# Kernel tuning notes

Measured on AMD Instinct MI355X. Metric: run time of the kernel, lower is better.

## Reference

```python
import jax, jax.numpy as jnp
import numpy as np

B, K, G = 1048576, 32, 8
SIGMA = 1.0


def setup_inputs() -> dict:
    key = jax.random.key(0)
    k1, k2 = jax.random.split(key)
    mu = jax.random.normal(k1, (B, K), dtype=jnp.float32)
    private_attribute = jax.random.randint(k2, (B,), 0, G, dtype=jnp.int64 if jax.config.jax_enable_x64 else jnp.int32)
    return {"mu": mu, "private_attribute": private_attribute}


def _gmm_loss(mu, labels):
    # --- segment reduce: per-label counts, means, covariances ---
    onehot = jax.nn.one_hot(labels, G, dtype=mu.dtype)          # [B,G]
    counts = jnp.sum(onehot, axis=0)                             # [G]
    mu_g = (onehot.T @ mu) / counts[:, None]                     # [G,K] group means
    diff = mu - mu_g[labels]                                     # [B,K] centered rows
    # Sigma_sum[g] = sum_{i in g} diff_i^T diff_i  (outer products)
    sigma_sum = jnp.einsum('bg,bi,bj->gij', onehot, diff, diff)  # [G,K,K]
    eye = jnp.eye(K, dtype=mu.dtype)
    sigma_g = SIGMA * eye + sigma_sum / counts[:, None, None]    # [G,K,K]

    # --- per-group inverse / logdet for Gaussian KL ---
    inv = jnp.linalg.inv(sigma_g)                                # [G,K,K]
    _, logdet = jnp.linalg.slogdet(sigma_g)                      # [G]

    # --- pairwise KL( N(u_i,S_i) || N(u_j,S_j) ) ---
    # tr(S_j^{-1} S_i)
    tr = jnp.einsum('jab,iba->ij', inv, sigma_g)                 # [G,G]
    d = mu_g[None, :, :] - mu_g[:, None, :]                      # d[i,j] = u_j - u_i
    mahal = jnp.einsum('ijd,jde,ije->ij', d, inv, d)             # [G,G]
    kl = 0.5 * (tr + mahal - K + logdet[None, :] - logdet[:, None])

    # original loop: for i in range(G-1): for j in range(1, G): if j != i
    idx = jnp.arange(G)
    mask = (idx[:, None] < G - 1) & (idx[None, :] >= 1) & (idx[:, None] != idx[None, :])
    w = counts[:, None] * counts[None, :]
    result = jnp.sum(jnp.where(mask, kl * w, jnp.zeros_like(kl)))
    return result / (float(B) ** 2)


def reference(mu, private_attribute):
    return _gmm_loss(mu, private_attribute)
```

## Files before the change

### kernel.cpp

```cpp
#include <hip/hip_runtime.h>
#include <math.h>

#define K 32
#define G 8
#define SIGMA_V 1.0f
#define RF __builtin_amdgcn_readfirstlane
#define RPB 512
#define RPW 128

#define RAW_OFF   0
#define MUSUM_OFF 8192
#define CNT_OFF   8448
#define ICNT_OFF  8456
#define CUR_OFF   8464
#define DESC_OFF  8480
#define IDX_OFF   16384
#define HDR_INTS  16384

#define WAITV(n) asm volatile("s_waitcnt vmcnt(" #n ")" ::: "memory")
typedef __attribute__((address_space(3))) void lds_void;
typedef __attribute__((address_space(1))) void glb_void;
#define GLL(gsrc, ldst) __builtin_amdgcn_global_load_lds((const glb_void*)(gsrc), (lds_void*)(ldst), 16, 0, 0)

__global__ __launch_bounds__(256, 8) void gmm_hist(const int* __restrict__ lab,
                                                   int* __restrict__ wsI, int B) {
  __shared__ int h[G];
  if (threadIdx.x < G) h[threadIdx.x] = 0;
  __syncthreads();
  int c[G];
  #pragma unroll
  for (int g = 0; g < G; ++g) c[g] = 0;
  const int nt = gridDim.x * blockDim.x;
  const int4* lab4 = reinterpret_cast<const int4*>(lab);
  for (int i = blockIdx.x * blockDim.x + threadIdx.x; i < B / 4; i += nt) {
    const int4 v = lab4[i];
    #pragma unroll
    for (int g = 0; g < G; ++g)
      c[g] += (v.x == g) + (v.y == g) + (v.z == g) + (v.w == g);
  }
  const int lane = threadIdx.x & 63;
  #pragma unroll
  for (int g = 0; g < G; ++g) {
    int t = c[g];
    #pragma unroll
    for (int off = 32; off >= 1; off >>= 1) t += __shfl_xor(t, off);
    if (lane == 0) atomicAdd(&h[g], t);
  }
  __syncthreads();
  if (threadIdx.x < G) atomicAdd(&wsI[ICNT_OFF + threadIdx.x], h[threadIdx.x]);
}

__global__ void gmm_prep(float* __restrict__ ws, int* __restrict__ wsI, int B, int nblk) {
  __shared__ int off[G], bb[G + 1], scnt[G];
  const int tid = threadIdx.x;
  if (tid == 0) {
    int o = 0, b = 0;
    for (int g = 0; g < G; ++g) {
      const int c = wsI[ICNT_OFF + g];
      scnt[g] = c; off[g] = o; bb[g] = b;
      ws[CNT_OFF + g] = (float)c;
      wsI[CUR_OFF + g] = o;
      o = (o + c + 15) & ~15;
      b += (c + RPB - 1) / RPB;
    }
    bb[G] = b;
  }
  __syncthreads();
  for (int t = tid; t < nblk; t += blockDim.x) {
    int st = 0, cn = 0, gg = 0;
    #pragma unroll
    for (int g = 0; g < G; ++g) {
      if (t >= bb[g] && t < bb[g + 1]) {
        const int k = t - bb[g];
        st = off[g] + k * RPB;
        const int rem = scnt[g] - k * RPB;
        cn = rem < RPB ? rem : RPB;
        gg = g;
      }
    }
    wsI[DESC_OFF + 3 * t]     = st;
    wsI[DESC_OFF + 3 * t + 1] = cn;
    wsI[DESC_OFF + 3 * t + 2] = gg;
  }
}

__global__ __launch_bounds__(256, 8) void gmm_scatter(const int* __restrict__ lab,
                                                      int* __restrict__ wsI, int B) {
  __shared__ int lcnt[G], lbase[G], lpos[G];
  const int tid = threadIdx.x;
  const int base = blockIdx.x * 1024;
  if (tid < G) { lcnt[tid] = 0; lpos[tid] = 0; }
  __syncthreads();
  const int4 v = *reinterpret_cast<const int4*>(lab + base + tid * 4);
  atomicAdd(&lcnt[v.x], 1); atomicAdd(&lcnt[v.y], 1);
  atomicAdd(&lcnt[v.z], 1); atomicAdd(&lcnt[v.w], 1);
  __syncthreads();
  if (tid < G) lbase[tid] = atomicAdd(&wsI[CUR_OFF + tid], lcnt[tid]);
  __syncthreads();
  int p;
  p = atomicAdd(&lpos[v.x], 1); wsI[IDX_OFF + lbase[v.x] + p] = base + tid * 4;
  p = atomicAdd(&lpos[v.y], 1); wsI[IDX_OFF + lbase[v.y] + p] = base + tid * 4 + 1;
  p = atomicAdd(&lpos[v.z], 1); wsI[IDX_OFF + lbase[v.z] + p] = base + tid * 4 + 2;
  p = atomicAdd(&lpos[v.w], 1); wsI[IDX_OFF + lbase[v.w] + p] = base + tid * 4 + 3;
}

#define OUTER(a, b) { \
  acc[0]=fmaf(a.x,b.x,acc[0]);   acc[1]=fmaf(a.x,b.y,acc[1]);   acc[2]=fmaf(a.x,b.z,acc[2]);   acc[3]=fmaf(a.x,b.w,acc[3]); \
  acc[4]=fmaf(a.y,b.x,acc[4]);   acc[5]=fmaf(a.y,b.y,acc[5]);   acc[6]=fmaf(a.y,b.z,acc[6]);   acc[7]=fmaf(a.y,b.w,acc[7]); \
  acc[8]=fmaf(a.z,b.x,acc[8]);   acc[9]=fmaf(a.z,b.y,acc[9]);   acc[10]=fmaf(a.z,b.z,acc[10]); acc[11]=fmaf(a.z,b.w,acc[11]); \
  acc[12]=fmaf(a.w,b.x,acc[12]); acc[13]=fmaf(a.w,b.y,acc[13]); acc[14]=fmaf(a.w,b.z,acc[14]); acc[15]=fmaf(a.w,b.w,acc[15]); \
  if (i8 == 0) { ms[0]+=b.x; ms[1]+=b.y; ms[2]+=b.z; ms[3]+=b.w; } }

#define STAGE(vlo, vhi, b) do { \
  float* db = &lds[wave * 1024 + (b) * 512]; \
  GLL(mu + (size_t)(unsigned)(vlo) * K + lf * 4, db); \
  GLL(mu + (size_t)(unsigned)(vhi) * K + lf * 4, db + 256); \
} while (0)

#define COMPUTE(b) do { \
  const float* sb = &lds[wave * 1024 + (b) * 512]; \
  _Pragma("unroll") \
  for (int r = 0; r < 16; ++r) { \
    const float4 a = *reinterpret_cast<const float4*>(&sb[r * 32 + i8 * 4]); \
    const float4 bv = *reinterpret_cast<const float4*>(&sb[r * 32 + j8 * 4]); \
    OUTER(a, bv); \
  } \
} while (0)

__global__ __launch_bounds__(256, 4) void gmm_stats3(const float* __restrict__ mu,
                                                     const int* __restrict__ wsI,
                                                     float* __restrict__ ws) {
  __shared__ float lds[4224];
  const int bd  = blockIdx.x * 3;
  const int s   = RF(wsI[DESC_OFF + bd]);
  const int cnt = RF(wsI[DESC_OFF + bd + 1]);
  const int g   = RF(wsI[DESC_OFF + bd + 2]);
  if (cnt <= 0) return;

  const int tid = threadIdx.x, wave = tid >> 6, lane = tid & 63;
  const int i8 = lane >> 3, j8 = lane & 7;
  const int lg = lane >> 3, lf = lane & 7;
  float acc[16], ms[4];
  #pragma unroll
  for (int e = 0; e < 16; ++e) acc[e] = 0.f;
  ms[0] = ms[1] = ms[2] = ms[3] = 0.f;

  int wcnt = cnt - wave * RPW;
  wcnt = wcnt < 0 ? 0 : (wcnt > RPW ? RPW : wcnt);
  const int* idxp = wsI + IDX_OFF + s + wave * RPW;

  const int nch = wcnt >> 4;
  int alo = 0, ahi = 0, slo = 0, shi = 0, tlo = 0, thi = 0;
  if (nch > 0) { alo = idxp[lg]; ahi = idxp[8 + lg]; }
  if (nch > 1) { slo = idxp[16 + lg]; shi = idxp[24 + lg]; }
  if (nch > 0) {
    if (nch > 1) WAITV(2); else WAITV(0);
    STAGE(alo, ahi, 0);
  }
  int buf = 0;
  for (int k = 0; k < nch; ++k) {
    const bool h1 = (k + 1) < nch, h2 = (k + 2) < nch;
    if (h2) { tlo = idxp[(k + 2) * 16 + lg]; thi = idxp[(k + 2) * 16 + 8 + lg]; }
    if (h1) {
      if (h2) { WAITV(4); } else { WAITV(2); }
      STAGE(slo, shi, buf ^ 1);
      if (h2) { WAITV(4); } else { WAITV(2); }
    } else {
      WAITV(0);
    }
    COMPUTE(buf);
    slo = tlo; shi = thi;
    buf ^= 1;
  }
  for (int q = nch << 4; q < wcnt; ++q) {
    const int r = idxp[q];
    const float* rp = mu + (size_t)(unsigned)r * K;
    const float4 a = *reinterpret_cast<const float4*>(rp + i8 * 4);
    const float4 bv = *reinterpret_cast<const float4*>(rp + j8 * 4);
    OUTER(a, bv);
  }

  __syncthreads();
  #pragma unroll
  for (int e = 0; e < 16; ++e) lds[wave * 1056 + e * 64 + lane] = acc[e];
  if (i8 == 0) {
    #pragma unroll
    for (int e = 0; e < 4; ++e) lds[wave * 1056 + 1024 + j8 * 4 + e] = ms[e];
  }
  __syncthreads();
  for (int t = tid; t < 1056; t += 256) {
    const float sm = lds[t] + lds[1056 + t] + lds[2112 + t] + lds[3168 + t];
    if (t < 1024) {
      const int e = t >> 6, ln = t & 63;
      const int row = 4 * (ln >> 3) + (e >> 2), col = 4 * (ln & 7) + (e & 3);
      atomicAdd(ws + RAW_OFF + g * K * K + row * K + col, sm);
    } else {
      atomicAdd(ws + MUSUM_OFF + g * K + (t - 1024), sm);
    }
  }
}

#define ACC_CASE(gc_, Av, Bv_) do{ \
  facc[gc_][0]=fmaf(Av.x,Bv_.x,facc[gc_][0]); facc[gc_][1]=fmaf(Av.x,Bv_.y,facc[gc_][1]); \
  facc[gc_][2]=fmaf(Av.y,Bv_.x,facc[gc_][2]); facc[gc_][3]=fmaf(Av.y,Bv_.y,facc[gc_][3]); \
  if (a_blk==0){ msum[gc_][0]+=Bv_.x; msum[gc_][1]+=Bv_.y; } }while(0)
#define PROC(gv, Av, Bv_) switch(gv){ \
  case 0: ACC_CASE(0,Av,Bv_); break; case 1: ACC_CASE(1,Av,Bv_); break; \
  case 2: ACC_CASE(2,Av,Bv_); break; case 3: ACC_CASE(3,Av,Bv_); break; \
  case 4: ACC_CASE(4,Av,Bv_); break; case 5: ACC_CASE(5,Av,Bv_); break; \
  case 6: ACC_CASE(6,Av,Bv_); break; default: ACC_CASE(7,Av,Bv_); break; }

__global__ __launch_bounds__(256, 4) void gmm_stats_fb(const float* __restrict__ mu,
                                                       const int* __restrict__ lab,
                                                       float* __restrict__ ws, int B) {
  const int tid = threadIdx.x;
  const int a_blk = tid >> 4, b_blk = tid & 15;
  const int rpb = B / 1024;
  const long rbase = (long)blockIdx.x * rpb;
  float facc[G][4]; float msum[G][2];
  #pragma unroll
  for (int g = 0; g < G; ++g) { facc[g][0]=facc[g][1]=facc[g][2]=facc[g][3]=0.f; msum[g][0]=msum[g][1]=0.f; }
  const float2* __restrict__ mu2 = reinterpret_cast<const float2*>(mu);
  for (int q = 0; q < rpb; ++q) {
    const long r = rbase + q;
    const float2 Av = mu2[r * 16 + a_blk];
    const float2 Bv_ = mu2[r * 16 + b_blk];
    const int g0 = RF(lab[r]);
    PROC(g0, Av, Bv_);
  }
  const int arow = a_blk * 2, bcol = b_blk * 2;
  #pragma unroll
  for (int g = 0; g < G; ++g) {
    float* base = &ws[RAW_OFF + g * K * K];
    atomicAdd(base + (arow)*K + bcol, facc[g][0]);
    atomicAdd(base + (arow)*K + bcol + 1, facc[g][1]);
    atomicAdd(base + (arow+1)*K + bcol, facc[g][2]);
    atomicAdd(base + (arow+1)*K + bcol + 1, facc[g][3]);
  }
  if (a_blk == 0)
    #pragma unroll
    for (int g = 0; g < G; ++g) {
      atomicAdd(&ws[MUSUM_OFF + g*K + bcol], msum[g][0]);
      atomicAdd(&ws[MUSUM_OFF + g*K + bcol + 1], msum[g][1]);
    }
}

__global__ __launch_bounds__(512, 1) void gmm_finalize(const float* __restrict__ ws,
                                                       float* __restrict__ out, int B) {
  __shared__ double sig[G][K][K];
  __shared__ double inv[G][K][K];
  __shared__ double mg[G][K];
  __shared__ double ldet[G];
  __shared__ double cshared[G];
  __shared__ double pairsum[G];
  const int tid = threadIdx.x;
  const int w = tid >> 6;
  const int lane = tid & 63;

  if (tid < G) cshared[tid] = (double)ws[CNT_OFF + tid];
  __syncthreads();
  const double cinv = 1.0 / cshared[w];
  if (lane < K) mg[w][lane] = (double)ws[MUSUM_OFF + w * K + lane] * cinv;
  __syncthreads();
  for (int e = lane; e < K * K; e += 64) {
    const int a = e >> 5, b = e & 31;
    double s = (double)ws[RAW_OFF + w * K * K + e] * cinv - mg[w][a] * mg[w][b];
    if (a == b) s += (double)SIGMA_V;
    sig[w][a][b] = s;
  }
  __syncthreads();

  const int c = lane & 31;
  double col[K];
  #pragma unroll
  for (int i2 = 0; i2 < K; ++i2) {
    double sv = sig[w][i2][c];
    col[i2] = (lane < K) ? sv : ((i2 == c) ? 1.0 : 0.0);
  }
  double ld = 0.0;
  #pragma unroll
  for (int j2 = 0; j2 < K; ++j2) {
    double rowj = col[j2];
    double p = __shfl(rowj, j2);
    double pinv = 1.0 / p;
    ld += log(p);
    double scaled = rowj * pinv;
    #pragma unroll
    for (int i2 = 0; i2 < K; ++i2) {
      if (i2 == j2) continue;
      double bij = __shfl(col[i2], j2);
      col[i2] = fma(-bij, scaled, col[i2]);
    }
    col[j2] = scaled;
  }
  if (lane >= K) {
    #pragma unroll
    for (int i2 = 0; i2 < K; ++i2) inv[w][i2][lane - K] = col[i2];
  }
  if (lane == 0) ldet[w] = ld;
  __syncthreads();

  double accp = 0.0;
  for (int jj = 0; jj < G; ++jj) {
    const bool ok = (w < G - 1) && (jj >= 1) && (w != jj);
    if (ok) {
      double t = 0.0;
      for (int e = lane; e < K * K; e += 64) {
        const int a = e >> 5, b = e & 31;
        const double da = mg[jj][a] - mg[w][a];
        const double db = mg[jj][b] - mg[w][b];
        t += inv[jj][a][b] * (sig[w][a][b] + da * db);
      }
      #pragma unroll
      for (int off = 32; off >= 1; off >>= 1) t += __shfl_xor(t, off);
      if (lane == 0) accp += 0.5 * (t - (double)K + ldet[jj] - ldet[w]) * cshared[w] * cshared[jj];
    }
  }
  if (lane == 0) pairsum[w] = accp;
  __syncthreads();
  if (tid == 0) {
    double tot = 0.0;
    #pragma unroll
    for (int q = 0; q < G; ++q) tot += pairsum[q];
    const double Bf = (double)B;
    out[0] = (float)(tot / (Bf * Bf));
  }
}

extern "C" void kernel_launch(void* const* d_in, const int* in_sizes, int n_in,
                              void* d_out, int out_size, void* d_ws, size_t ws_size,
                              hipStream_t stream) {
  const float* mu = (const float*)d_in[0];
  const int* lab = (const int*)d_in[1];
  float* ws = (float*)d_ws;
  int* wsI = (int*)d_ws;
  float* out = (float*)d_out;
  const int B = in_sizes[1];

  hipMemsetAsync(d_ws, 0, (size_t)DESC_OFF * 4, stream);
  hipLaunchKernelGGL(gmm_hist, dim3(256), dim3(256), 0, stream, lab, wsI, B);

  const size_t need = (size_t)(HDR_INTS + B + 16 * G + 32) * 4;
  if (ws_size >= need) {
    const int nblk = (B + RPB - 1) / RPB + G;
    hipLaunchKernelGGL(gmm_prep, dim3(1), dim3(256), 0, stream, ws, wsI, B, nblk);
    hipLaunchKernelGGL(gmm_scatter, dim3(B / 1024), dim3(256), 0, stream, lab, wsI, B);
    hipLaunchKernelGGL(gmm_stats3, dim3(nblk), dim3(256), 0, stream, mu, wsI, ws);
  } else {
    hipLaunchKernelGGL(gmm_prep, dim3(1), dim3(256), 0, stream, ws, wsI, B, 0);
    hipLaunchKernelGGL(gmm_stats_fb, dim3(1024), dim3(256), 0, stream, mu, lab, ws, B);
  }
  hipLaunchKernelGGL(gmm_finalize, dim3(1), dim3(512), 0, stream, ws, out, B);
}
```

Baseline: 209.9 us.

## Fuse prep into histogram, locally sort scatter output, deepen stats pipeline

The single-block prep kernel is folded into the histogram kernel: the last block to finish, found with an atomic done counter, computes offsets and block descriptors, which removes one launch. The scatter kernel now sorts indices per group in LDS before writing, so global writes are contiguous runs instead of random single stores. The stats kernel switches to 8-row chunks with a 4-deep global_load_lds ring buffer on the full-chunk path and accumulates mean sums in every lane rather than only i8==0. The partial-chunk path now waits on each load before using it, which serialises loads, and the change in ms accumulation has to stay consistent with how those sums are reduced later.

Result: slower. 219.0 us (+4.3%).

```diff
diff --git a/kernel.cpp b/kernel.cpp
--- a/kernel.cpp
+++ b/kernel.cpp
@@ -13,6 +13,7 @@
 #define CNT_OFF   8448
 #define ICNT_OFF  8456
 #define CUR_OFF   8464
+#define DONE_OFF  8472
 #define DESC_OFF  8480
 #define IDX_OFF   16384
 #define HDR_INTS  16384
@@ -23,45 +24,52 @@
 #define GLL(gsrc, ldst) __builtin_amdgcn_global_load_lds((const glb_void*)(gsrc), (lds_void*)(ldst), 16, 0, 0)
 
 __global__ __launch_bounds__(256, 8) void gmm_hist(const int* __restrict__ lab,
-                                                   int* __restrict__ wsI, int B) {
+                                                   float* __restrict__ ws,
+                                                   int* __restrict__ wsI, int B, int nblk) {
   __shared__ int h[G];
-  if (threadIdx.x < G) h[threadIdx.x] = 0;
+  __shared__ int amLast;
+  __shared__ int off[G], bb[G + 1], scnt[G];
+  const int tid = threadIdx.x;
+  if (tid < G) h[tid] = 0;
   __syncthreads();
   int c[G];
   #pragma unroll
   for (int g = 0; g < G; ++g) c[g] = 0;
   const int nt = gridDim.x * blockDim.x;
   const int4* lab4 = reinterpret_cast<const int4*>(lab);
-  for (int i = blockIdx.x * blockDim.x + threadIdx.x; i < B / 4; i += nt) {
+  for (int i = blockIdx.x * blockDim.x + tid; i < B / 4; i += nt) {
     const int4 v = lab4[i];
     #pragma unroll
     for (int g = 0; g < G; ++g)
       c[g] += (v.x == g) + (v.y == g) + (v.z == g) + (v.w == g);
   }
-  const int lane = threadIdx.x & 63;
+  const int lane = tid & 63;
   #pragma unroll
   for (int g = 0; g < G; ++g) {
     int t = c[g];
     #pragma unroll
-    for (int off = 32; off >= 1; off >>= 1) t += __shfl_xor(t, off);
+    for (int o = 32; o >= 1; o >>= 1) t += __shfl_xor(t, o);
     if (lane == 0) atomicAdd(&h[g], t);
   }
   __syncthreads();
-  if (threadIdx.x < G) atomicAdd(&wsI[ICNT_OFF + threadIdx.x], h[threadIdx.x]);
-}
-
-__global__ void gmm_prep(float* __restrict__ ws, int* __restrict__ wsI, int B, int nblk) {
-  __shared__ int off[G], bb[G + 1], scnt[G];
-  const int tid = threadIdx.x;
+  if (tid < G) atomicAdd(&wsI[ICNT_OFF + tid], h[tid]);
+  __syncthreads();
+  if (tid == 0) {
+    __threadfence();
+    amLast = (atomicAdd(&wsI[DONE_OFF], 1) == (int)gridDim.x - 1);
+  }
+  __syncthreads();
+  if (!amLast) return;
+
   if (tid == 0) {
     int o = 0, b = 0;
     for (int g = 0; g < G; ++g) {
-      const int c = wsI[ICNT_OFF + g];
-      scnt[g] = c; off[g] = o; bb[g] = b;
-      ws[CNT_OFF + g] = (float)c;
+      const int cc = atomicAdd(&wsI[ICNT_OFF + g], 0);
+      scnt[g] = cc; off[g] = o; bb[g] = b;
+      ws[CNT_OFF + g] = (float)cc;
       wsI[CUR_OFF + g] = o;
-      o = (o + c + 15) & ~15;
-      b += (c + RPB - 1) / RPB;
+      o = (o + cc + 15) & ~15;
+      b += (cc + RPB - 1) / RPB;
     }
     bb[G] = b;
   }
@@ -86,7 +94,8 @@
 
 __global__ __launch_bounds__(256, 8) void gmm_scatter(const int* __restrict__ lab,
                                                       int* __restrict__ wsI, int B) {
-  __shared__ int lcnt[G], lbase[G], lpos[G];
+  __shared__ int lcnt[G], lofs[G + 1], lbase[G], lpos[G];
+  __shared__ int sorted[1024];
   const int tid = threadIdx.x;
   const int base = blockIdx.x * 1024;
   if (tid < G) { lcnt[tid] = 0; lpos[tid] = 0; }
@@ -95,13 +104,27 @@
   atomicAdd(&lcnt[v.x], 1); atomicAdd(&lcnt[v.y], 1);
   atomicAdd(&lcnt[v.z], 1); atomicAdd(&lcnt[v.w], 1);
   __syncthreads();
+  if (tid == 0) {
+    int o = 0;
+    #pragma unroll
+    for (int g = 0; g < G; ++g) { lofs[g] = o; o += lcnt[g]; }
+    lofs[G] = o;
+  }
+  __syncthreads();
   if (tid < G) lbase[tid] = atomicAdd(&wsI[CUR_OFF + tid], lcnt[tid]);
-  __syncthreads();
   int p;
-  p = atomicAdd(&lpos[v.x], 1); wsI[IDX_OFF + lbase[v.x] + p] = base + tid * 4;
-  p = atomicAdd(&lpos[v.y], 1); wsI[IDX_OFF + lbase[v.y] + p] = base + tid * 4 + 1;
-  p = atomicAdd(&lpos[v.z], 1); wsI[IDX_OFF + lbase[v.z] + p] = base + tid * 4 + 2;
-  p = atomicAdd(&lpos[v.w], 1); wsI[IDX_OFF + lbase[v.w] + p] = base + tid * 4 + 3;
+  p = atomicAdd(&lpos[v.x], 1); sorted[lofs[v.x] + p] = base + tid * 4;
+  p = atomicAdd(&lpos[v.y], 1); sorted[lofs[v.y] + p] = base + tid * 4 + 1;
+  p = atomicAdd(&lpos[v.z], 1); sorted[lofs[v.z] + p] = base + tid * 4 + 2;
+  p = atomicAdd(&lpos[v.w], 1); sorted[lofs[v.w] + p] = base + tid * 4 + 3;
+  __syncthreads();
+  for (int e = tid; e < 1024; e += 256) {
+    const int val = sorted[e];
+    int gg = 0;
+    #pragma unroll
+    for (int g = 1; g < G; ++g) gg += (e >= lofs[g]);
+    wsI[IDX_OFF + lbase[gg] + (e - lofs[gg])] = val;
+  }
 }
 
 #define OUTER(a, b) { \
@@ -109,19 +132,18 @@
   acc[4]=fmaf(a.y,b.x,acc[4]);   acc[5]=fmaf(a.y,b.y,acc[5]);   acc[6]=fmaf(a.y,b.z,acc[6]);   acc[7]=fmaf(a.y,b.w,acc[7]); \
   acc[8]=fmaf(a.z,b.x,acc[8]);   acc[9]=fmaf(a.z,b.y,acc[9]);   acc[10]=fmaf(a.z,b.z,acc[10]); acc[11]=fmaf(a.z,b.w,acc[11]); \
   acc[12]=fmaf(a.w,b.x,acc[12]); acc[13]=fmaf(a.w,b.y,acc[13]); acc[14]=fmaf(a.w,b.z,acc[14]); acc[15]=fmaf(a.w,b.w,acc[15]); \
-  if (i8 == 0) { ms[0]+=b.x; ms[1]+=b.y; ms[2]+=b.z; ms[3]+=b.w; } }
-
-#define STAGE(vlo, vhi, b) do { \
-  float* db = &lds[wave * 1024 + (b) * 512]; \
-  GLL(mu + (size_t)(unsigned)(vlo) * K + lf * 4, db); \
-  GLL(mu + (size_t)(unsigned)(vhi) * K + lf * 4, db + 256); \
+  ms[0]+=b.x; ms[1]+=b.y; ms[2]+=b.z; ms[3]+=b.w; }
+
+#define STAGE8(iv, bi) do { \
+  float* db = &lds[wave * 1024 + (bi) * 256]; \
+  GLL(mu + (size_t)(unsigned)(iv) * K + lf * 4, db); \
 } while (0)
 
-#define COMPUTE(b) do { \
-  const float* sb = &lds[wave * 1024 + (b) * 512]; \
+#define COMPUTE8(bi) do { \
+  const float* sb = &lds[wave * 1024 + (bi) * 256]; \
   _Pragma("unroll") \
-  for (int r = 0; r < 16; ++r) { \
-    const float4 a = *reinterpret_cast<const float4*>(&sb[r * 32 + i8 * 4]); \
+  for (int r = 0; r < 8; ++r) { \
+    const float4 a  = *reinterpret_cast<const float4*>(&sb[r * 32 + i8 * 4]); \
     const float4 bv = *reinterpret_cast<const float4*>(&sb[r * 32 + j8 * 4]); \
     OUTER(a, bv); \
   } \
@@ -139,7 +161,7 @@
 
   const int tid = threadIdx.x, wave = tid >> 6, lane = tid & 63;
   const int i8 = lane >> 3, j8 = lane & 7;
-  const int lg = lane >> 3, lf = lane & 7;
+  const int lg8 = lane >> 3, lf = lane & 7;
   float acc[16], ms[4];
   #pragma unroll
   for (int e = 0; e < 16; ++e) acc[e] = 0.f;
@@ -148,34 +170,46 @@
   int wcnt = cnt - wave * RPW;
   wcnt = wcnt < 0 ? 0 : (wcnt > RPW ? RPW : wcnt);
   const int* idxp = wsI + IDX_OFF + s + wave * RPW;
-
-  const int nch = wcnt >> 4;
-  int alo = 0, ahi = 0, slo = 0, shi = 0, tlo = 0, thi = 0;
-  if (nch > 0) { alo = idxp[lg]; ahi = idxp[8 + lg]; }
-  if (nch > 1) { slo = idxp[16 + lg]; shi = idxp[24 + lg]; }
-  if (nch > 0) {
-    if (nch > 1) WAITV(2); else WAITV(0);
-    STAGE(alo, ahi, 0);
-  }
-  int buf = 0;
-  for (int k = 0; k < nch; ++k) {
-    const bool h1 = (k + 1) < nch, h2 = (k + 2) < nch;
-    if (h2) { tlo = idxp[(k + 2) * 16 + lg]; thi = idxp[(k + 2) * 16 + 8 + lg]; }
-    if (h1) {
-      if (h2) { WAITV(4); } else { WAITV(2); }
-      STAGE(slo, shi, buf ^ 1);
-      if (h2) { WAITV(4); } else { WAITV(2); }
-    } else {
-      WAITV(0);
-    }
-    COMPUTE(buf);
-    slo = tlo; shi = thi;
-    buf ^= 1;
-  }
-  for (int q = nch << 4; q < wcnt; ++q) {
+  const int nch = wcnt >> 3;
+
+  if (nch == 16) {
+    const int i0 = idxp[lg8];
+    int inext    = idxp[8 + lg8];
+    WAITV(1); STAGE8(i0, 0);
+    {
+      const int i1 = inext;
+      inext = idxp[16 + lg8];
+      WAITV(2); STAGE8(i1, 1);
+    }
+    {
+      const int i2 = inext;
+      inext = idxp[24 + lg8];
+      WAITV(2); STAGE8(i2, 2);
+    }
+    #pragma unroll 1
+    for (int k = 0; k < 12; ++k) {
+      const int istage = inext;
+      inext = idxp[(k + 4) * 8 + lg8];
+      WAITV(2);
+      STAGE8(istage, (k + 3) & 3);
+      COMPUTE8(k & 3);
+    }
+    WAITV(1); STAGE8(inext, 15 & 3);
+    COMPUTE8(12 & 3);
+    COMPUTE8(13 & 3);
+    WAITV(1); COMPUTE8(14 & 3);
+    WAITV(0); COMPUTE8(15 & 3);
+  } else {
+    for (int k = 0; k < nch; ++k) {
+      const int iv = idxp[k * 8 + lg8];
+      WAITV(0); STAGE8(iv, k & 3);
+      WAITV(0); COMPUTE8(k & 3);
+    }
+  }
+  for (int q = nch << 3; q < wcnt; ++q) {
     const int r = idxp[q];
     const float* rp = mu + (size_t)(unsigned)r * K;
-    const float4 a = *reinterpret_cast<const float4*>(rp + i8 * 4);
+    const float4 a  = *reinterpret_cast<const float4*>(rp + i8 * 4);
     const float4 bv = *reinterpret_cast<const float4*>(rp + j8 * 4);
     OUTER(a, bv);
   }
@@ -338,16 +372,15 @@
   const int B = in_sizes[1];
 
   hipMemsetAsync(d_ws, 0, (size_t)DESC_OFF * 4, stream);
-  hipLaunchKernelGGL(gmm_hist, dim3(256), dim3(256), 0, stream, lab, wsI, B);
 
   const size_t need = (size_t)(HDR_INTS + B + 16 * G + 32) * 4;
   if (ws_size >= need) {
     const int nblk = (B + RPB - 1) / RPB + G;
-    hipLaunchKernelGGL(gmm_prep, dim3(1), dim3(256), 0, stream, ws, wsI, B, nblk);
+    hipLaunchKernelGGL(gmm_hist, dim3(256), dim3(256), 0, stream, lab, ws, wsI, B, nblk);
     hipLaunchKernelGGL(gmm_scatter, dim3(B / 1024), dim3(256), 0, stream, lab, wsI, B);
     hipLaunchKernelGGL(gmm_stats3, dim3(nblk), dim3(256), 0, stream, mu, wsI, ws);
   } else {
-    hipLaunchKernelGGL(gmm_prep, dim3(1), dim3(256), 0, stream, ws, wsI, B, 0);
+    hipLaunchKernelGGL(gmm_hist, dim3(256), dim3(256), 0, stream, lab, ws, wsI, B, 0);
     hipLaunchKernelGGL(gmm_stats_fb, dim3(1024), dim3(256), 0, stream, mu, lab, ws, B);
   }
   hipLaunchKernelGGL(gmm_finalize, dim3(1), dim3(512), 0, stream, ws, out, B);
```
